# Performance work log

Measured on AMD Instinct MI355X. Metric: run time of the kernel, lower is better.

## Reference

```python
import jax, jax.numpy as jnp
import numpy as np

B, S, D, DM, H, DH, DF, L, T = 4096, 64, 256, 512, 4, 64, 512, 6, 20


def mish(x):
    return x * jnp.tanh(jax.nn.softplus(x))


def layernorm(x, eps=1e-5):
    mu = jnp.mean(x, axis=-1, keepdims=True)
    var = jnp.var(x, axis=-1, keepdims=True)
    return (x - mu) * jax.lax.rsqrt(var + eps)


def setup_inputs() -> dict:
    key = jax.random.key(0)
    ks = iter(jax.random.split(key, 32))
    w = lambda *shape: jax.random.normal(next(ks), shape, dtype=jnp.float32) * 0.02
    inp = {
        'x_t': jax.random.normal(next(ks), (B, S, D), dtype=jnp.float32),
        't': jax.random.randint(next(ks), (B,), 0, T + 1),
        'backbone_latent': jax.random.normal(next(ks), (B, S, DM), dtype=jnp.float32),
        # timestep embedding
        'emb': w(T + 1, D),
        'te_w1': w(D, 4 * D), 'te_b1': jnp.zeros((4 * D,), jnp.float32),
        'te_w2': w(4 * D, D), 'te_b2': jnp.zeros((D,), jnp.float32),
        # cond projection
        'cp_w1': w(DM, D), 'cp_b1': jnp.zeros((D,), jnp.float32),
        'cp_w2': w(D, D), 'cp_b2': jnp.zeros((D,), jnp.float32),
        # stacked per-layer DiT block params [L, ...]
        'adaln_w': w(L, D, 6 * D), 'adaln_b': jnp.zeros((L, 6 * D), jnp.float32),
        'qkv_w': w(L, D, 3 * D), 'qkv_b': jnp.zeros((L, 3 * D), jnp.float32),
        'op_w': w(L, D, D), 'op_b': jnp.zeros((L, D), jnp.float32),
        'ffn_w1': w(L, D, DF), 'ffn_b1': jnp.zeros((L, DF), jnp.float32),
        'ffn_w2': w(L, DF, D), 'ffn_b2': jnp.zeros((L, D), jnp.float32),
        # final adaLN + projection (random here for nontrivial test, zero-init in original)
        'fa_w': w(D, 2 * D), 'fa_b': jnp.zeros((2 * D,), jnp.float32),
        'fp_w': w(D, D), 'fp_b': jnp.zeros((D,), jnp.float32),
    }
    return inp


def _forward(x_t, t, backbone_latent, emb, te_w1, te_b1, te_w2, te_b2,
             cp_w1, cp_b1, cp_w2, cp_b2, adaln_w, adaln_b, qkv_w, qkv_b,
             op_w, op_b, ffn_w1, ffn_b1, ffn_w2, ffn_b2, fa_w, fa_b, fp_w, fp_b):
    # conditioning vector c: [B, D]
    te = emb[t]                                   # [B, D]
    te = mish(te @ te_w1 + te_b1) @ te_w2 + te_b2
    cond = jnp.mean(backbone_latent, axis=1)      # [B, DM]
    cond = mish(cond @ cp_w1 + cp_b1) @ cp_w2 + cp_b2
    c = te + cond
    mc = mish(c)

    x = x_t
    for l in range(L):
        mod = (mc @ adaln_w[l] + adaln_b[l])[:, None, :]   # [B, 1, 6D]
        sh1, sc1, g1, sh2, sc2, g2 = jnp.split(mod, 6, axis=-1)
        # attention sub-block
        h = layernorm(x) * (1.0 + sc1) + sh1
        qkv = (h @ qkv_w[l] + qkv_b[l]).reshape(B, S, 3, H, DH)
        q = qkv[:, :, 0].transpose(0, 2, 1, 3)   # [B, H, S, DH]
        k = qkv[:, :, 1].transpose(0, 2, 1, 3)
        v = qkv[:, :, 2].transpose(0, 2, 1, 3)
        attn = jax.nn.softmax(jnp.einsum('bhsd,bhtd->bhst', q, k) * DH ** -0.5, axis=-1)
        h = jnp.einsum('bhst,bhtd->bhsd', attn, v).transpose(0, 2, 1, 3).reshape(B, S, D)
        h = h @ op_w[l] + op_b[l]
        x = x + g1 * h
        # FFN sub-block
        h = layernorm(x) * (1.0 + sc2) + sh2
        h = mish(h @ ffn_w1[l] + ffn_b1[l]) @ ffn_w2[l] + ffn_b2[l]
        x = x + g2 * h

    mod = (mc @ fa_w + fa_b)[:, None, :]
    shift, scale = jnp.split(mod, 2, axis=-1)
    x = layernorm(x) * (1.0 + scale) + shift
    return x @ fp_w + fp_b


def reference(x_t, t, backbone_latent, emb, te_w1, te_b1, te_w2, te_b2,
              cp_w1, cp_b1, cp_w2, cp_b2, adaln_w, adaln_b, qkv_w, qkv_b,
              op_w, op_b, ffn_w1, ffn_b1, ffn_w2, ffn_b2, fa_w, fa_b, fp_w, fp_b):
    return _forward(x_t, t, backbone_latent, emb, te_w1, te_b1, te_w2, te_b2,
                    cp_w1, cp_b1, cp_w2, cp_b2, adaln_w, adaln_b, qkv_w, qkv_b,
                    op_w, op_b, ffn_w1, ffn_b1, ffn_w2, ffn_b2, fa_w, fa_b, fp_w, fp_b)
```

## Files before the change

kernel.cpp:

```cpp
#include <hip/hip_runtime.h>

typedef unsigned short u16;
typedef float f32x4 __attribute__((ext_vector_type(4)));
typedef __bf16 bf16x8 __attribute__((ext_vector_type(8)));

__device__ __forceinline__ u16 f2b(float f) {
  unsigned u = __builtin_bit_cast(unsigned, f);
  u += 0x7FFF + ((u >> 16) & 1);
  return (u16)(u >> 16);
}

__device__ __forceinline__ float b2f(u16 v) {
  unsigned u = (unsigned)v << 16;
  return __builtin_bit_cast(float, u);
}

__device__ __forceinline__ f32x4 ld_bf4(const u16* p) {
  ushort4 v = *(const ushort4*)p;
  f32x4 r;
  r[0] = b2f(v.x); r[1] = b2f(v.y); r[2] = b2f(v.z); r[3] = b2f(v.w);
  return r;
}

__device__ __forceinline__ float mishf(float x) {
// ... 271 lines not shown
      f32x4 xn = x + g4 * (acc[mt][nt] + b4);
      acc[mt][nt] = xn;
      s1[mt] += xn[0] + xn[1] + xn[2] + xn[3];
      s2[mt] += xn[0] * xn[0] + xn[1] * xn[1] + xn[2] * xn[2] + xn[3] * xn[3];
    }
  }
#pragma unroll
  for (int mt = 0; mt < 4; ++mt) {
    s1[mt] += __shfl_xor(s1[mt], 16); s1[mt] += __shfl_xor(s1[mt], 32);
    s2[mt] += __shfl_xor(s2[mt], 16); s2[mt] += __shfl_xor(s2[mt], 32);
  }
  float* st = (float*)&As[0][0];
  if (lane < 16) {
#pragma unroll
    for (int mt = 0; mt < 4; ++mt) {
      st[wave * 128 + mt * 16 + lane] = s1[mt];
      st[wave * 128 + 64 + mt * 16 + lane] = s2[mt];
    }
  }
  __syncthreads();
  float mean[4], rstd[4];
#pragma unroll
  for (int mt = 0; mt < 4; ++mt) {
    float a = 0.f, q = 0.f;
#pragma unroll
    for (int w2 = 0; w2 < 4; ++w2) {
      a += st[w2 * 128 + mt * 16 + rl];
      q += st[w2 * 128 + 64 + mt * 16 + rl];
    }
    mean[mt] = a * (1.f / 256.f);
    float var = q * (1.f / 256.f) - mean[mt] * mean[mt];
    rstd[mt] = rsqrtf(fmaxf(var, 0.f) + 1e-5f);
  }
#pragma unroll
  for (int nt = 0; nt < 4; ++nt) {
    const int col = wc + nt * 16 + c4;
    const f32x4 sc4 = ld_bf4(lnsc + b * lnstride + col);
    const f32x4 sh4 = ld_bf4(lnsh + b * lnstride + col);
#pragma unroll
    for (int mt = 0; mt < 4; ++mt) {
      const long row = tm + mt * 16 + rl;
      ushort4 xo;
      xo.x = f2b(acc[mt][nt][0]); xo.y = f2b(acc[mt][nt][1]);
      xo.z = f2b(acc[mt][nt][2]); xo.w = f2b(acc[mt][nt][3]);
      *(ushort4*)(xout + row * 256 + col) = xo;
      f32x4 h = (acc[mt][nt] - mean[mt]) * rstd[mt] * (1.f + sc4) + sh4;
      ushort4 o;
      o.x = f2b(h[0]); o.y = f2b(h[1]); o.z = f2b(h[2]); o.w = f2b(h[3]);
      *(ushort4*)(hout + row * 256 + col) = o;
    }
  }
}

__global__ __launch_bounds__(512)
void ffn_fused(const u16* __restrict__ xln, const u16* __restrict__ W1t,
               const float* __restrict__ b1, const u16* __restrict__ W2t,
               const float* __restrict__ b2, const u16* __restrict__ xres,
               const u16* __restrict__ gptr,
               const u16* __restrict__ lnsh, const u16* __restrict__ lnsc, int lnstride,
               u16* __restrict__ xout, u16* __restrict__ hout) {
  __shared__ __align__(16) u16 Ax[64 * 256];
  __shared__ __align__(16) u16 Ws[2][256 * 64];
  __shared__ __align__(16) u16 H1[64 * 512];
  const int tid = threadIdx.x, lane = tid & 63, wave = tid >> 6;
  const long b = blockIdx.x;
  const int rl = lane & 15;
  const int c4 = (lane >> 4) << 2;
  const int kq = lane >> 4;

  {
    const u16* src = xln + b * (64 * 256);
#pragma unroll
    for (int i = 0; i < 4; ++i) {
      int c = tid + (i << 9);
      int r = c >> 5, cc = c & 31;
      int sch = (cc & ~7) | ((cc & 7) ^ (r & 7));
      gl_lds16(src + r * 256 + (sch << 3), &Ax[c << 3]);
    }
  }
  auto stageW = [&](const u16* Wsrc, int Kw, int R0, int k0, int buf) {
#pragma unroll
    for (int i = 0; i < 4; ++i) {
      int c = tid + (i << 9);
      int r = c >> 3;
      int sch = (c & 7) ^ (r & 7);
      gl_lds16(Wsrc + (long)(R0 + r) * Kw + k0 + (sch << 3), &Ws[buf][c << 3]);
    }
  };
  stageW(W1t, 256, 0, 0, 0);
  __syncthreads();

  int cur = 0;
  for (int nh = 0; nh < 2; ++nh) {
    f32x4 acc[4][2] = {};
    for (int t = 0; t < 4; ++t) {
      int s = nh * 4 + t;
      if (s < 7) stageW(W1t, 256, ((s + 1) >> 2) * 256, ((s + 1) & 3) * 64, cur ^ 1);
      else stageW(W2t, 512, 0, 0, cur ^ 1);
#pragma unroll
      for (int kt = 0; kt < 2; ++kt) {
        bf16x8 av[4], bv[2];
#pragma unroll
        for (int mt = 0; mt < 4; ++mt) {
          int r = mt * 16 + rl;
          int kc = t * 8 + kt * 4 + kq;
          int slot = (kc & ~7) | ((kc & 7) ^ (r & 7));
          av[mt] = ldb8(&Ax[r * 256 + (slot << 3)]);
        }
#pragma unroll
        for (int nf = 0; nf < 2; ++nf) {
          int wr_ = wave * 32 + nf * 16 + rl;
          int slot = (kt * 4 + kq) ^ (wr_ & 7);
          bv[nf] = ldb8(&Ws[cur][wr_ * 64 + (slot << 3)]);
        }
#pragma unroll
        for (int mt = 0; mt < 4; ++mt)
#pragma unroll
          for (int nf = 0; nf < 2; ++nf)
            acc[mt][nf] = __builtin_amdgcn_mfma_f32_16x16x32_bf16(bv[nf], av[mt], acc[mt][nf], 0, 0, 0);
      }
      __syncthreads();
      cur ^= 1;
    }
#pragma unroll
    for (int nf = 0; nf < 2; ++nf) {
      const int col = nh * 256 + wave * 32 + nf * 16 + c4;
      const f32x4 bb = *(const f32x4*)(b1 + col);
      const int c8 = col >> 3;
      const int sub = (col & 7) << 1;
#pragma unroll
      for (int mt = 0; mt < 4; ++mt) {
        const int r = mt * 16 + rl;
        f32x4 v = acc[mt][nf] + bb;
        ushort4 o;
        o.x = f2b(mishf(v[0])); o.y = f2b(mishf(v[1]));
        o.z = f2b(mishf(v[2])); o.w = f2b(mishf(v[3]));
        int slot = (c8 & ~7) | ((c8 & 7) ^ (r & 7));
        *(ushort4*)((char*)H1 + r * 1024 + (slot << 4) + sub) = o;
      }
    }
  }
  __syncthreads();

  f32x4 acc[4][2] = {};
  for (int t = 0; t < 8; ++t) {
    if (t < 7) stageW(W2t, 512, 0, (t + 1) * 64, cur ^ 1);
#pragma unroll
    for (int kt = 0; kt < 2; ++kt) {
      bf16x8 av[4], bv[2];
#pragma unroll
      for (int mt = 0; mt < 4; ++mt) {
        int r = mt * 16 + rl;
        int kc = t * 8 + kt * 4 + kq;
        int slot = (kc & ~7) | ((kc & 7) ^ (r & 7));
        av[mt] = ldb8((const u16*)((const char*)H1 + r * 1024 + (slot << 4)));
      }
#pragma unroll
      for (int nf = 0; nf < 2; ++nf) {
        int wr_ = wave * 32 + nf * 16 + rl;
        int slot = (kt * 4 + kq) ^ (wr_ & 7);
        bv[nf] = ldb8(&Ws[cur][wr_ * 64 + (slot << 3)]);
      }
#pragma unroll
      for (int mt = 0; mt < 4; ++mt)
#pragma unroll
        for (int nf = 0; nf < 2; ++nf)
          acc[mt][nf] = __builtin_amdgcn_mfma_f32_16x16x32_bf16(bv[nf], av[mt], acc[mt][nf], 0, 0, 0);
    }
    __syncthreads();
    cur ^= 1;
  }
  float s1[4] = {}, s2[4] = {};
#pragma unroll
  for (int nf = 0; nf < 2; ++nf) {
    const int col = wave * 32 + nf * 16 + c4;
    const f32x4 bb = *(const f32x4*)(b2 + col);
    const f32x4 g4 = ld_bf4(gptr + b * 1536 + col);
#pragma unroll
    for (int mt = 0; mt < 4; ++mt) {
      const long row = b * 64 + mt * 16 + rl;
      f32x4 x = ld_bf4(xres + row * 256 + col);
      f32x4 xn = x + g4 * (acc[mt][nf] + bb);
      acc[mt][nf] = xn;
      s1[mt] += xn[0] + xn[1] + xn[2] + xn[3];
      s2[mt] += xn[0] * xn[0] + xn[1] * xn[1] + xn[2] * xn[2] + xn[3] * xn[3];
    }
  }
#pragma unroll
  for (int mt = 0; mt < 4; ++mt) {
    s1[mt] += __shfl_xor(s1[mt], 16); s1[mt] += __shfl_xor(s1[mt], 32);
    s2[mt] += __shfl_xor(s2[mt], 16); s2[mt] += __shfl_xor(s2[mt], 32);
  }
  float* st = (float*)&Ax[0];
  if (lane < 16) {
#pragma unroll
    for (int mt = 0; mt < 4; ++mt) {
      st[wave * 128 + mt * 16 + lane] = s1[mt];
      st[wave * 128 + 64 + mt * 16 + lane] = s2[mt];
    }
  }
  __syncthreads();
  float mean[4], rstd[4];
#pragma unroll
  for (int mt = 0; mt < 4; ++mt) {
    float a = 0.f, q = 0.f;
#pragma unroll
    for (int w2 = 0; w2 < 8; ++w2) {
      a += st[w2 * 128 + mt * 16 + rl];
      q += st[w2 * 128 + 64 + mt * 16 + rl];
    }
    mean[mt] = a * (1.f / 256.f);
    float var = q * (1.f / 256.f) - mean[mt] * mean[mt];
    rstd[mt] = rsqrtf(fmaxf(var, 0.f) + 1e-5f);
  }
#pragma unroll
  for (int nf = 0; nf < 2; ++nf) {
    const int col = wave * 32 + nf * 16 + c4;
    const f32x4 sc4 = ld_bf4(lnsc + b * lnstride + col);
    const f32x4 sh4 = ld_bf4(lnsh + b * lnstride + col);
#pragma unroll
    for (int mt = 0; mt < 4; ++mt) {
      const long row = b * 64 + mt * 16 + rl;
      ushort4 xo;
      xo.x = f2b(acc[mt][nf][0]); xo.y = f2b(acc[mt][nf][1]);
      xo.z = f2b(acc[mt][nf][2]); xo.w = f2b(acc[mt][nf][3]);
      *(ushort4*)(xout + row * 256 + col) = xo;
      f32x4 h = (acc[mt][nf] - mean[mt]) * rstd[mt] * (1.f + sc4) + sh4;
      ushort4 o;
      o.x = f2b(h[0]); o.y = f2b(h[1]); o.z = f2b(h[2]); o.w = f2b(h[3]);
      *(ushort4*)(hout + row * 256 + col) = o;
    }
  }
}

__global__ __launch_bounds__(128)
void attn_kernel(const u16* __restrict__ qkv, u16* __restrict__ out) {
  __shared__ __align__(16) u16 vt_s[2][64 * 72];
  __shared__ __align__(16) u16 p_s[2][64 * 72];
  const int lane = threadIdx.x & 63;
  const int wave = threadIdx.x >> 6;
  const long b = blockIdx.x >> 1;
  const int h = ((blockIdx.x & 1) << 1) | wave;
  u16* vt = vt_s[wave];
  u16* pl = p_s[wave];
  const u16* base = qkv + b * (64 * 768);
#pragma unroll
  for (int it = 0; it < 8; ++it) {
    int chunk = it * 64 + lane;
    int t = chunk >> 3, dhb = (chunk & 7) << 3;
    union { uint4 u; u16 s[8]; } uv;
    uv.u = *(const uint4*)(base + t * 768 + 512 + h * 64 + dhb);
#pragma unroll
    for (int j = 0; j < 8; ++j) vt[(dhb + j) * 72 + t] = uv.s[j];
  }
  const u16* qb = base + h * 64;
  const u16* kb = base + 256 + h * 64;
  f32x4 sacc[4][4] = {};
#pragma unroll
  for (int kt = 0; kt < 2; ++kt) {
    bf16x8 qa[4], kv[4];
#pragma unroll
    for (int mt = 0; mt < 4; ++mt)
      qa[mt] = ldb8(qb + ((lane & 15) + mt * 16) * 768 + kt * 32 + ((lane >> 4) << 3));
#pragma unroll
    for (int nt = 0; nt < 4; ++nt)
      kv[nt] = ldb8(kb + ((lane & 15) + nt * 16) * 768 + kt * 32 + ((lane >> 4) << 3));
#pragma unroll
    for (int mt = 0; mt < 4; ++mt)
#pragma unroll
      for (int nt = 0; nt < 4; ++nt)
        sacc[mt][nt] = __builtin_amdgcn_mfma_f32_16x16x32_bf16(qa[mt], kv[nt], sacc[mt][nt], 0, 0, 0);
  }
  const float scale = 0.125f;
#pragma unroll
  for (int mt = 0; mt < 4; ++mt) {
#pragma unroll
    for (int r = 0; r < 4; ++r) {
      float mx = fmaxf(fmaxf(sacc[mt][0][r], sacc[mt][1][r]), fmaxf(sacc[mt][2][r], sacc[mt][3][r]));
#pragma unroll
      for (int m = 1; m <= 8; m <<= 1) mx = fmaxf(mx, __shfl_xor(mx, m));
      float p[4];
      float sum = 0.f;
#pragma unroll
      for (int nt = 0; nt < 4; ++nt) { p[nt] = __expf((sacc[mt][nt][r] - mx) * scale); sum += p[nt]; }
#pragma unroll
      for (int m = 1; m <= 8; m <<= 1) sum += __shfl_xor(sum, m);
      const float rinv = 1.f / sum;
      const int s = mt * 16 + ((lane >> 4) << 2) + r;
#pragma unroll
      for (int nt = 0; nt < 4; ++nt) pl[s * 72 + nt * 16 + (lane & 15)] = f2b(p[nt] * rinv);
    }
  }
  __syncthreads();
  f32x4 oacc[4][4] = {};
#pragma unroll
  for (int kt = 0; kt < 2; ++kt) {
    bf16x8 pa[4], vv[4];
#pragma unroll
    for (int mt = 0; mt < 4; ++mt)
      pa[mt] = ldb8(pl + ((lane & 15) + mt * 16) * 72 + kt * 32 + ((lane >> 4) << 3));
#pragma unroll
    for (int nt = 0; nt < 4; ++nt)
      vv[nt] = ldb8(vt + ((lane & 15) + nt * 16) * 72 + kt * 32 + ((lane >> 4) << 3));
#pragma unroll
    for (int mt = 0; mt < 4; ++mt)
#pragma unroll
      for (int nt = 0; nt < 4; ++nt)
        oacc[mt][nt] = __builtin_amdgcn_mfma_f32_16x16x32_bf16(vv[nt], pa[mt], oacc[mt][nt], 0, 0, 0);
  }
  u16* ob = out + b * (64 * 256) + h * 64;
#pragma unroll
  for (int mt = 0; mt < 4; ++mt)
#pragma unroll
    for (int nt = 0; nt < 4; ++nt) {
      const int s = mt * 16 + (lane & 15);
      const int d4 = nt * 16 + ((lane >> 4) << 2);
      ushort4 o;
      o.x = f2b(oacc[mt][nt][0]); o.y = f2b(oacc[mt][nt][1]);
      o.z = f2b(oacc[mt][nt][2]); o.w = f2b(oacc[mt][nt][3]);
      *(ushort4*)(ob + s * 256 + d4) = o;
    }
}

extern "C" void kernel_launch(void* const* d_in, const int* in_sizes, int n_in,
                              void* d_out, int out_size, void* d_ws, size_t ws_size,
                              hipStream_t stream) {
  (void)in_sizes; (void)n_in; (void)out_size; (void)ws_size;
  const int B = 4096, L = 6;
  const long BSr = (long)B * 64;

  const float* x_t = (const float*)d_in[0];
  const int* tvec = (const int*)d_in[1];
  const float* backbone = (const float*)d_in[2];
  const float* emb = (const float*)d_in[3];
  const float* te_w1 = (const float*)d_in[4];
  const float* te_b1 = (const float*)d_in[5];
  const float* te_w2 = (const float*)d_in[6];
  const float* te_b2 = (const float*)d_in[7];
  const float* cp_w1 = (const float*)d_in[8];
  const float* cp_b1 = (const float*)d_in[9];
  const float* cp_w2 = (const float*)d_in[10];
  const float* cp_b2 = (const float*)d_in[11];
  const float* adaln_w = (const float*)d_in[12];
  const float* adaln_b = (const float*)d_in[13];
  const float* qkv_w = (const float*)d_in[14];
  const float* qkv_b = (const float*)d_in[15];
  const float* op_w = (const float*)d_in[16];
  const float* op_b = (const float*)d_in[17];
  const float* ffn_w1 = (const float*)d_in[18];
  const float* ffn_b1 = (const float*)d_in[19];
  const float* ffn_w2 = (const float*)d_in[20];
  const float* ffn_b2 = (const float*)d_in[21];
  const float* fa_w = (const float*)d_in[22];
  const float* fa_b = (const float*)d_in[23];
  const float* fp_w = (const float*)d_in[24];
  const float* fp_b = (const float*)d_in[25];

  char* w = (char*)d_ws;
  auto alloc = [&](size_t bytes) { char* p = w; w += (bytes + 255) & ~(size_t)255; return p; };
  u16* WT_cp1 = (u16*)alloc(256L * 512 * 2);
  u16* WT_cp2 = (u16*)alloc(256L * 256 * 2);
  u16* WT_adaln = (u16*)alloc(6L * 1536 * 256 * 2);
  u16* WT_qkv = (u16*)alloc(6L * 768 * 256 * 2);
  u16* WT_op = (u16*)alloc(6L * 256 * 256 * 2);
  u16* WT_f1 = (u16*)alloc(6L * 512 * 256 * 2);
  u16* WT_f2 = (u16*)alloc(6L * 256 * 512 * 2);
  u16* WT_fa = (u16*)alloc(512L * 256 * 2);
  u16* WT_fp = (u16*)alloc(256L * 256 * 2);
  float* te_tab = (float*)alloc(21L * 256 * 4);
  u16* cond = (u16*)alloc(4096L * 512 * 2);
  u16* c1 = (u16*)alloc(4096L * 256 * 2);
  u16* mc = (u16*)alloc(4096L * 256 * 2);
  u16* modb6 = (u16*)alloc(6L * 4096 * 1536 * 2);
  u16* famod = (u16*)alloc(4096L * 512 * 2);
  u16* hbuf = (u16*)alloc(BSr * 256 * 2);
  u16* qkvbuf = (u16*)alloc(BSr * 768 * 2);
  u16* xbuf = (u16*)d_out;

  transpose_w<<<dim3(4, 8, 1), 256, 0, stream>>>(cp_w1, WT_cp1, 512, 256);
  transpose_w<<<dim3(4, 4, 1), 256, 0, stream>>>(cp_w2, WT_cp2, 256, 256);
  transpose_w<<<dim3(24, 4, 6), 256, 0, stream>>>(adaln_w, WT_adaln, 256, 1536);
  transpose_w<<<dim3(12, 4, 6), 256, 0, stream>>>(qkv_w, WT_qkv, 256, 768);
  transpose_w<<<dim3(4, 4, 6), 256, 0, stream>>>(op_w, WT_op, 256, 256);
  transpose_w<<<dim3(8, 4, 6), 256, 0, stream>>>(ffn_w1, WT_f1, 256, 512);
  transpose_w<<<dim3(4, 8, 6), 256, 0, stream>>>(ffn_w2, WT_f2, 512, 256);
  transpose_w<<<dim3(8, 4, 1), 256, 0, stream>>>(fa_w, WT_fa, 256, 512);
  transpose_w<<<dim3(4, 4, 1), 256, 0, stream>>>(fp_w, WT_fp, 256, 256);

  te_table_kernel<<<21, 1024, 0, stream>>>(emb, te_w1, te_b1, te_w2, te_b2, te_tab);
  cond_mean_kernel<<<4096, 256, 0, stream>>>(backbone, cond);

  gemm_bt<1><<<dim3(2, 32), 256, 0, stream>>>(cond, WT_cp1, cp_b1, c1, nullptr, nullptr, 4096, 256, 512);
  gemm_bt<4><<<dim3(2, 32), 256, 0, stream>>>(c1, WT_cp2, cp_b2, mc, tvec, te_tab, 4096, 256, 256);
  gemm_bt<0><<<dim3(4, 32), 256, 0, stream>>>(mc, WT_fa, fa_b, famod, nullptr, nullptr, 4096, 512, 256);
  for (int l = 0; l < L; ++l)
    gemm_bt<0><<<dim3(12, 32), 256, 0, stream>>>(mc, WT_adaln + (long)l * 1536 * 256, adaln_b + l * 1536,
                                                 modb6 + (long)l * 4096 * 1536, nullptr, nullptr, 4096, 1536, 256);

  ln_mod<<<BSr / 4, 256, 0, stream>>>(x_t, modb6, 1536, 0, 256, hbuf);

  for (int l = 0; l < L; ++l) {
    const u16* mb = modb6 + (long)l * 4096 * 1536;
    gemm_bt<0><<<dim3(6, BSr / 128), 256, 0, stream>>>(hbuf, WT_qkv + (long)l * 768 * 256, qkv_b + l * 768,
                                                       qkvbuf, nullptr, nullptr, (int)BSr, 768, 256);
    attn_kernel<<<B * 2, 128, 0, stream>>>(qkvbuf, hbuf);
    if (l == 0)
      gemm_ln<256, true><<<BSr / 64, 256, 0, stream>>>(hbuf, WT_op, op_b, x_t, mb + 512,
                                                       mb + 768, mb + 1024, 1536, xbuf, hbuf);
    else
      gemm_ln<256, false><<<BSr / 64, 256, 0, stream>>>(hbuf, WT_op + (long)l * 256 * 256, op_b + l * 256,
                                                        xbuf, mb + 512, mb + 768, mb + 1024, 1536, xbuf, hbuf);
    const u16* nsh = (l < 5) ? (modb6 + (long)(l + 1) * 4096 * 1536) : famod;
    const u16* nsc = (l < 5) ? (modb6 + (long)(l + 1) * 4096 * 1536 + 256) : (famod + 256);
    const int nstride = (l < 5) ? 1536 : 512;
    ffn_fused<<<B, 512, 0, stream>>>(hbuf, WT_f1 + (long)l * 512 * 256, ffn_b1 + l * 512,
                                     WT_f2 + (long)l * 256 * 512, ffn_b2 + l * 256,
                                     xbuf, mb + 1280, nsh, nsc, nstride, xbuf, hbuf);
  }
  gemm_bt<3><<<dim3(2, BSr / 128), 256, 0, stream>>>(hbuf, WT_fp, fp_b, d_out, nullptr, nullptr, (int)BSr, 256, 256);
}
```

Measured before the change: 6.485 ms.

## Fuse QKV projection with attention and retile FFN to 32-row blocks

Adds a qkv_attn kernel that computes the QKV projection for two heads of one batch element straight into shared memory and then runs softmax attention there. This removes the qkvbuf round trip through global memory and one launch per layer. The FFN kernel is also restructured to handle 32 rows per 256-thread block with a single-buffered weight tile, doubling the grid and cutting shared memory use so more blocks can be resident. The cost is that each QKV block re-reads the input rows, the attention path leaves two of six waves idle, and weight staging in the FFN no longer overlaps with compute.

```diff
diff --git a/kernel.cpp b/kernel.cpp
--- a/kernel.cpp
+++ b/kernel.cpp
@@ -347,274 +347,354 @@
   }
 }
 
-__global__ __launch_bounds__(512)
+__global__ __launch_bounds__(384)
+void qkv_attn(const u16* __restrict__ xln, const u16* __restrict__ Wq,
+              const float* __restrict__ qbias, u16* __restrict__ aout) {
+  __shared__ __align__(16) u16 Wlds[384 * 32];
+  __shared__ __align__(16) u16 QP[2][64 * 64];
+  __shared__ __align__(16) u16 Kl[2][64 * 64];
+  __shared__ __align__(16) u16 Vt[128 * 64];
+  const int tid = threadIdx.x, lane = tid & 63, wave = tid >> 6;
+  const long b = blockIdx.x >> 1;
+  const int hp = blockIdx.x & 1;
+  const int rl = lane & 15, kq = lane >> 4, c4 = kq << 2;
+  const u16* xg = xln + b * (64 * 256);
+
+  f32x4 acc[4][4] = {};
+  for (int t = 0; t < 8; ++t) {
+    {
+      const int k0 = t << 5;
+#pragma unroll
+      for (int i = 0; i < 4; ++i) {
+        int c = tid + i * 384;
+        int r = c >> 2, kcl = c & 3;
+        int sch = kcl ^ ((r >> 1) & 3);
+        long rg = (long)((r >> 7) * 256 + hp * 128 + (r & 127));
+        gl_lds16(Wq + rg * 256 + k0 + (sch << 3), &Wlds[c << 3]);
+      }
+    }
+    __syncthreads();
+    bf16x8 av[4], bv[4];
+#pragma unroll
+    for (int mt = 0; mt < 4; ++mt)
+      av[mt] = ldb8(xg + (mt * 16 + rl) * 256 + (t << 5) + (kq << 3));
+#pragma unroll
+    for (int nt = 0; nt < 4; ++nt) {
+      const int wr_ = (wave << 6) + nt * 16 + rl;
+      const int slot = kq ^ ((wr_ >> 1) & 3);
+      bv[nt] = ldb8(&Wlds[(wr_ << 5) + (slot << 3)]);
+    }
+    if (wave < 4) {
+#pragma unroll
+      for (int mt = 0; mt < 4; ++mt)
+#pragma unroll
+        for (int nt = 0; nt < 4; ++nt)
+          acc[mt][nt] = __builtin_amdgcn_mfma_f32_16x16x32_bf16(bv[nt], av[mt], acc[mt][nt], 0, 0, 0);
+    } else {
+#pragma unroll
+      for (int mt = 0; mt < 4; ++mt)
+#pragma unroll
+        for (int nt = 0; nt < 4; ++nt)
+          acc[mt][nt] = __builtin_amdgcn_mfma_f32_16x16x32_bf16(av[mt], bv[nt], acc[mt][nt], 0, 0, 0);
+    }
+    __syncthreads();
+  }
+  if (wave < 4) {
+    const int head = wave & 1;
+    u16* dst = (wave >> 1) ? Kl[head] : QP[head];
+#pragma unroll
+    for (int nt = 0; nt < 4; ++nt) {
+      const int dh = nt * 16 + c4;
+      const int gc = (wave >> 1) * 256 + hp * 128 + (wave & 1) * 64 + dh;
+      const f32x4 bb = *(const f32x4*)(qbias + gc);
+      const int c16 = dh >> 3, sub = (dh & 7) << 1;
+#pragma unroll
+      for (int mt = 0; mt < 4; ++mt) {
+        const int tok = mt * 16 + rl;
+        f32x4 v = acc[mt][nt] + bb;
+        ushort4 o;
+        o.x = f2b(v[0]); o.y = f2b(v[1]); o.z = f2b(v[2]); o.w = f2b(v[3]);
+        const int slot = c16 ^ (tok & 7);
+        *(ushort4*)((char*)dst + tok * 128 + (slot << 4) + sub) = o;
+      }
+    }
+  } else {
+#pragma unroll
+    for (int nt = 0; nt < 4; ++nt) {
+      const int dh = ((wave - 4) << 6) + nt * 16 + rl;
+      const float bb = qbias[512 + hp * 128 + dh];
+#pragma unroll
+      for (int mt = 0; mt < 4; ++mt) {
+        const int tok = mt * 16 + c4;
+        f32x4 v = acc[mt][nt] + bb;
+        ushort4 o;
+        o.x = f2b(v[0]); o.y = f2b(v[1]); o.z = f2b(v[2]); o.w = f2b(v[3]);
+        const int c16 = tok >> 3, sub = (tok & 7) << 1;
+        const int slot = c16 ^ (dh & 7);
+        *(ushort4*)((char*)Vt + dh * 128 + (slot << 4) + sub) = o;
+      }
+    }
+  }
+  __syncthreads();
+
+  const int ah = wave >> 1, arow = (wave & 1) << 5;
+  f32x4 sacc[2][4] = {};
+  if (wave < 4) {
+#pragma unroll
+    for (int kt = 0; kt < 2; ++kt) {
+      const int kc = kt * 4 + kq;
+      bf16x8 qa[2], kv[4];
+#pragma unroll
+      for (int mt = 0; mt < 2; ++mt) {
+        const int q = arow + mt * 16 + rl;
+        qa[mt] = ldb8((const u16*)((char*)QP[ah] + q * 128 + ((kc ^ (q & 7)) << 4)));
+      }
+#pragma unroll
+      for (int nt = 0; nt < 4; ++nt) {
+        const int tt = nt * 16 + rl;
+        kv[nt] = ldb8((const u16*)((char*)Kl[ah] + tt * 128 + ((kc ^ (tt & 7)) << 4)));
+      }
+#pragma unroll
+      for (int mt = 0; mt < 2; ++mt)
+#pragma unroll
+        for (int nt = 0; nt < 4; ++nt)
+          sacc[mt][nt] = __builtin_amdgcn_mfma_f32_16x16x32_bf16(kv[nt], qa[mt], sacc[mt][nt], 0, 0, 0);
+    }
+  }
+  __syncthreads();
+  if (wave < 4) {
+    const float scale = 0.125f;
+#pragma unroll
+    for (int mt = 0; mt < 2; ++mt) {
+      float mx = -1e30f;
+#pragma unroll
+      for (int nt = 0; nt < 4; ++nt)
+#pragma unroll
+        for (int j = 0; j < 4; ++j) mx = fmaxf(mx, sacc[mt][nt][j]);
+      mx = fmaxf(mx, __shfl_xor(mx, 16));
+      mx = fmaxf(mx, __shfl_xor(mx, 32));
+      float sum = 0.f;
+      f32x4 p[4];
+#pragma unroll
+      for (int nt = 0; nt < 4; ++nt)
+#pragma unroll
+        for (int j = 0; j < 4; ++j) { p[nt][j] = __expf((sacc[mt][nt][j] - mx) * scale); sum += p[nt][j]; }
+      sum += __shfl_xor(sum, 16);
+      sum += __shfl_xor(sum, 32);
+      const float rinv = 1.f / sum;
+      const int q = arow + mt * 16 + rl;
+#pragma unroll
+      for (int nt = 0; nt < 4; ++nt) {
+        const int tcol = nt * 16 + c4;
+        ushort4 o;
+        o.x = f2b(p[nt][0] * rinv); o.y = f2b(p[nt][1] * rinv);
+        o.z = f2b(p[nt][2] * rinv); o.w = f2b(p[nt][3] * rinv);
+        const int slot = (tcol >> 3) ^ (q & 7);
+        *(ushort4*)((char*)QP[ah] + q * 128 + (slot << 4) + ((tcol & 7) << 1)) = o;
+      }
+    }
+  }
+  __syncthreads();
+  if (wave < 4) {
+    f32x4 oacc[2][4] = {};
+#pragma unroll
+    for (int kt = 0; kt < 2; ++kt) {
+      const int kc = kt * 4 + kq;
+      bf16x8 pa[2], vv[4];
+#pragma unroll
+      for (int mt = 0; mt < 2; ++mt) {
+        const int q = arow + mt * 16 + rl;
+        pa[mt] = ldb8((const u16*)((char*)QP[ah] + q * 128 + ((kc ^ (q & 7)) << 4)));
+      }
+#pragma unroll
+      for (int nt = 0; nt < 4; ++nt) {
+        const int dh = (ah << 6) + nt * 16 + rl;
+        vv[nt] = ldb8((const u16*)((char*)Vt + dh * 128 + ((kc ^ (dh & 7)) << 4)));
+      }
+#pragma unroll
+      for (int mt = 0; mt < 2; ++mt)
+#pragma unroll
+        for (int nt = 0; nt < 4; ++nt)
+          oacc[mt][nt] = __builtin_amdgcn_mfma_f32_16x16x32_bf16(vv[nt], pa[mt], oacc[mt][nt], 0, 0, 0);
+    }
+    u16* ob = aout + b * (64 * 256) + (hp * 2 + ah) * 64;
+#pragma unroll
+    for (int mt = 0; mt < 2; ++mt)
+#pragma unroll
+      for (int nt = 0; nt < 4; ++nt) {
+        const int q = arow + mt * 16 + rl;
+        const int dh = nt * 16 + c4;
+        ushort4 o;
+        o.x = f2b(oacc[mt][nt][0]); o.y = f2b(oacc[mt][nt][1]);
+        o.z = f2b(oacc[mt][nt][2]); o.w = f2b(oacc[mt][nt][3]);
+        *(ushort4*)(ob + q * 256 + dh) = o;
+      }
+  }
+}
+
+__global__ __launch_bounds__(256)
 void ffn_fused(const u16* __restrict__ xln, const u16* __restrict__ W1t,
                const float* __restrict__ b1, const u16* __restrict__ W2t,
                const float* __restrict__ b2, const u16* __restrict__ xres,
                const u16* __restrict__ gptr,
                const u16* __restrict__ lnsh, const u16* __restrict__ lnsc, int lnstride,
                u16* __restrict__ xout, u16* __restrict__ hout) {
-  __shared__ __align__(16) u16 Ax[64 * 256];
-  __shared__ __align__(16) u16 Ws[2][256 * 64];
-  __shared__ __align__(16) u16 H1[64 * 512];
+  __shared__ __align__(16) u16 Ax[32 * 256];
+  __shared__ __align__(16) u16 Ws[256 * 64];
+  __shared__ __align__(16) u16 H1[32 * 512];
   const int tid = threadIdx.x, lane = tid & 63, wave = tid >> 6;
-  const long b = blockIdx.x;
-  const int rl = lane & 15;
-  const int c4 = (lane >> 4) << 2;
-  const int kq = lane >> 4;
+  const long blk = blockIdx.x;
+  const long b = blk >> 1;
+  const long row0 = blk << 5;
+  const int rl = lane & 15, kq = lane >> 4, c4 = kq << 2;
 
   {
-    const u16* src = xln + b * (64 * 256);
+    const u16* src = xln + row0 * 256;
 #pragma unroll
     for (int i = 0; i < 4; ++i) {
-      int c = tid + (i << 9);
+      int c = tid + (i << 8);
       int r = c >> 5, cc = c & 31;
       int sch = (cc & ~7) | ((cc & 7) ^ (r & 7));
       gl_lds16(src + r * 256 + (sch << 3), &Ax[c << 3]);
     }
   }
-  auto stageW = [&](const u16* Wsrc, int Kw, int R0, int k0, int buf) {
-#pragma unroll
-    for (int i = 0; i < 4; ++i) {
-      int c = tid + (i << 9);
+  auto stageW = [&](int s) {
+    const u16* Wsrc; int Kw, R0, k0;
+    if (s < 8) { Wsrc = W1t; Kw = 256; R0 = (s >> 2) << 8; k0 = (s & 3) << 6; }
+    else       { Wsrc = W2t; Kw = 512; R0 = 0;             k0 = (s - 8) << 6; }
+#pragma unroll
+    for (int i = 0; i < 8; ++i) {
+      int c = tid + (i << 8);
       int r = c >> 3;
       int sch = (c & 7) ^ (r & 7);
-      gl_lds16(Wsrc + (long)(R0 + r) * Kw + k0 + (sch << 3), &Ws[buf][c << 3]);
+      gl_lds16(Wsrc + (long)(R0 + r) * Kw + k0 + (sch << 3), &Ws[c << 3]);
     }
   };
-  stageW(W1t, 256, 0, 0, 0);
-  __syncthreads();
-
-  int cur = 0;
-  for (int nh = 0; nh < 2; ++nh) {
-    f32x4 acc[4][2] = {};
-    for (int t = 0; t < 4; ++t) {
-      int s = nh * 4 + t;
-      if (s < 7) stageW(W1t, 256, ((s + 1) >> 2) * 256, ((s + 1) & 3) * 64, cur ^ 1);
-      else stageW(W2t, 512, 0, 0, cur ^ 1);
-#pragma unroll
-      for (int kt = 0; kt < 2; ++kt) {
-        bf16x8 av[4], bv[2];
-#pragma unroll
-        for (int mt = 0; mt < 4; ++mt) {
-          int r = mt * 16 + rl;
-          int kc = t * 8 + kt * 4 + kq;
-          int slot = (kc & ~7) | ((kc & 7) ^ (r & 7));
-          av[mt] = ldb8(&Ax[r * 256 + (slot << 3)]);
+  stageW(0);
+  __syncthreads();
+
+  f32x4 acc[2][4] = {};
+  for (int s = 0; s < 16; ++s) {
+#pragma unroll
+    for (int kt = 0; kt < 2; ++kt) {
+      bf16x8 av[2], bv[4];
+      if (s < 8) {
+        const int kc = (s & 3) * 8 + kt * 4 + kq;
+#pragma unroll
+        for (int mt = 0; mt < 2; ++mt) {
+          const int r = mt * 16 + rl;
+          const int slot = (kc & ~7) | ((kc & 7) ^ (r & 7));
+          av[mt] = ldb8(&Ax[(r << 8) + (slot << 3)]);
         }
-#pragma unroll
-        for (int nf = 0; nf < 2; ++nf) {
-          int wr_ = wave * 32 + nf * 16 + rl;
-          int slot = (kt * 4 + kq) ^ (wr_ & 7);
-          bv[nf] = ldb8(&Ws[cur][wr_ * 64 + (slot << 3)]);
+      } else {
+        const int kc = (s - 8) * 8 + kt * 4 + kq;
+#pragma unroll
+        for (int mt = 0; mt < 2; ++mt) {
+          const int r = mt * 16 + rl;
+          const int slot = (kc & ~7) | ((kc & 7) ^ (r & 7));
+          av[mt] = ldb8(&H1[(r << 9) + (slot << 3)]);
         }
-#pragma unroll
-        for (int mt = 0; mt < 4; ++mt)
-#pragma unroll
-          for (int nf = 0; nf < 2; ++nf)
-            acc[mt][nf] = __builtin_amdgcn_mfma_f32_16x16x32_bf16(bv[nf], av[mt], acc[mt][nf], 0, 0, 0);
-      }
-      __syncthreads();
-      cur ^= 1;
-    }
-#pragma unroll
-    for (int nf = 0; nf < 2; ++nf) {
-      const int col = nh * 256 + wave * 32 + nf * 16 + c4;
-      const f32x4 bb = *(const f32x4*)(b1 + col);
-      const int c8 = col >> 3;
-      const int sub = (col & 7) << 1;
-#pragma unroll
-      for (int mt = 0; mt < 4; ++mt) {
-        const int r = mt * 16 + rl;
-        f32x4 v = acc[mt][nf] + bb;
-        ushort4 o;
-        o.x = f2b(mishf(v[0])); o.y = f2b(mishf(v[1]));
-        o.z = f2b(mishf(v[2])); o.w = f2b(mishf(v[3]));
-        int slot = (c8 & ~7) | ((c8 & 7) ^ (r & 7));
-        *(ushort4*)((char*)H1 + r * 1024 + (slot << 4) + sub) = o;
-      }
-    }
-  }
-  __syncthreads();
-
-  f32x4 acc[4][2] = {};
-  for (int t = 0; t < 8; ++t) {
-    if (t < 7) stageW(W2t, 512, 0, (t + 1) * 64, cur ^ 1);
-#pragma unroll
-    for (int kt = 0; kt < 2; ++kt) {
-      bf16x8 av[4], bv[2];
-#pragma unroll
-      for (int mt = 0; mt < 4; ++mt) {
-        int r = mt * 16 + rl;
-        int kc = t * 8 + kt * 4 + kq;
-        int slot = (kc & ~7) | ((kc & 7) ^ (r & 7));
-        av[mt] = ldb8((const u16*)((const char*)H1 + r * 1024 + (slot << 4)));
-      }
-#pragma unroll
-      for (int nf = 0; nf < 2; ++nf) {
-        int wr_ = wave * 32 + nf * 16 + rl;
-        int slot = (kt * 4 + kq) ^ (wr_ & 7);
-        bv[nf] = ldb8(&Ws[cur][wr_ * 64 + (slot << 3)]);
-      }
-#pragma unroll
-      for (int mt = 0; mt < 4; ++mt)
-#pragma unroll
-        for (int nf = 0; nf < 2; ++nf)
-          acc[mt][nf] = __builtin_amdgcn_mfma_f32_16x16x32_bf16(bv[nf], av[mt], acc[mt][nf], 0, 0, 0);
+      }
+#pragma unroll
+      for (int nt = 0; nt < 4; ++nt) {
+        const int wr_ = (wave << 6) + nt * 16 + rl;
+        const int slot = (kt * 4 + kq) ^ (wr_ & 7);
+        bv[nt] = ldb8(&Ws[(wr_ << 6) + (slot << 3)]);
+      }
+#pragma unroll
+      for (int mt = 0; mt < 2; ++mt)
+#pragma unroll
+        for (int nt = 0; nt < 4; ++nt)
+          acc[mt][nt] = __builtin_amdgcn_mfma_f32_16x16x32_bf16(bv[nt], av[mt], acc[mt][nt], 0, 0, 0);
     }
     __syncthreads();
-    cur ^= 1;
-  }
-  float s1[4] = {}, s2[4] = {};
-#pragma unroll
-  for (int nf = 0; nf < 2; ++nf) {
-    const int col = wave * 32 + nf * 16 + c4;
+    if (s == 3 || s == 7) {
+      const int nh = s >> 2;
+#pragma unroll
+      for (int nt = 0; nt < 4; ++nt) {
+        const int col = (nh << 8) + (wave << 6) + nt * 16 + c4;
+        const f32x4 bb = *(const f32x4*)(b1 + col);
+        const int c16 = col >> 3, sub = (col & 7) << 1;
+#pragma unroll
+        for (int mt = 0; mt < 2; ++mt) {
+          const int r = mt * 16 + rl;
+          f32x4 v = acc[mt][nt] + bb;
+          ushort4 o;
+          o.x = f2b(mishf(v[0])); o.y = f2b(mishf(v[1]));
+          o.z = f2b(mishf(v[2])); o.w = f2b(mishf(v[3]));
+          const int slot = (c16 & ~7) | ((c16 & 7) ^ (r & 7));
+          *(ushort4*)((char*)H1 + r * 1024 + (slot << 4) + sub) = o;
+        }
+      }
+#pragma unroll
+      for (int mt = 0; mt < 2; ++mt)
+#pragma unroll
+        for (int nt = 0; nt < 4; ++nt) acc[mt][nt] = (f32x4){0.f, 0.f, 0.f, 0.f};
+    }
+    if (s < 15) { stageW(s + 1); __syncthreads(); }
+  }
+
+  float s1[2] = {}, s2[2] = {};
+#pragma unroll
+  for (int nt = 0; nt < 4; ++nt) {
+    const int col = (wave << 6) + nt * 16 + c4;
     const f32x4 bb = *(const f32x4*)(b2 + col);
     const f32x4 g4 = ld_bf4(gptr + b * 1536 + col);
 #pragma unroll
-    for (int mt = 0; mt < 4; ++mt) {
-      const long row = b * 64 + mt * 16 + rl;
+    for (int mt = 0; mt < 2; ++mt) {
+      const long row = row0 + mt * 16 + rl;
       f32x4 x = ld_bf4(xres + row * 256 + col);
-      f32x4 xn = x + g4 * (acc[mt][nf] + bb);
-      acc[mt][nf] = xn;
+      f32x4 xn = x + g4 * (acc[mt][nt] + bb);
+      acc[mt][nt] = xn;
       s1[mt] += xn[0] + xn[1] + xn[2] + xn[3];
       s2[mt] += xn[0] * xn[0] + xn[1] * xn[1] + xn[2] * xn[2] + xn[3] * xn[3];
     }
   }
 #pragma unroll
-  for (int mt = 0; mt < 4; ++mt) {
+  for (int mt = 0; mt < 2; ++mt) {
     s1[mt] += __shfl_xor(s1[mt], 16); s1[mt] += __shfl_xor(s1[mt], 32);
     s2[mt] += __shfl_xor(s2[mt], 16); s2[mt] += __shfl_xor(s2[mt], 32);
   }
   float* st = (float*)&Ax[0];
   if (lane < 16) {
 #pragma unroll
-    for (int mt = 0; mt < 4; ++mt) {
-      st[wave * 128 + mt * 16 + lane] = s1[mt];
-      st[wave * 128 + 64 + mt * 16 + lane] = s2[mt];
-    }
-  }
-  __syncthreads();
-  float mean[4], rstd[4];
-#pragma unroll
-  for (int mt = 0; mt < 4; ++mt) {
+    for (int mt = 0; mt < 2; ++mt) {
+      st[wave * 64 + mt * 16 + lane] = s1[mt];
+      st[256 + wave * 64 + mt * 16 + lane] = s2[mt];
+    }
+  }
+  __syncthreads();
+  float mean[2], rstd[2];
+#pragma unroll
+  for (int mt = 0; mt < 2; ++mt) {
     float a = 0.f, q = 0.f;
 #pragma unroll
-    for (int w2 = 0; w2 < 8; ++w2) {
-      a += st[w2 * 128 + mt * 16 + rl];
-      q += st[w2 * 128 + 64 + mt * 16 + rl];
+    for (int w2 = 0; w2 < 4; ++w2) {
+      a += st[w2 * 64 + mt * 16 + rl];
+      q += st[256 + w2 * 64 + mt * 16 + rl];
     }
     mean[mt] = a * (1.f / 256.f);
     float var = q * (1.f / 256.f) - mean[mt] * mean[mt];
     rstd[mt] = rsqrtf(fmaxf(var, 0.f) + 1e-5f);
   }
 #pragma unroll
-  for (int nf = 0; nf < 2; ++nf) {
-    const int col = wave * 32 + nf * 16 + c4;
+  for (int nt = 0; nt < 4; ++nt) {
+    const int col = (wave << 6) + nt * 16 + c4;
     const f32x4 sc4 = ld_bf4(lnsc + b * lnstride + col);
     const f32x4 sh4 = ld_bf4(lnsh + b * lnstride + col);
 #pragma unroll
-    for (int mt = 0; mt < 4; ++mt) {
-      const long row = b * 64 + mt * 16 + rl;
+    for (int mt = 0; mt < 2; ++mt) {
+      const long row = row0 + mt * 16 + rl;
       ushort4 xo;
-      xo.x = f2b(acc[mt][nf][0]); xo.y = f2b(acc[mt][nf][1]);
-      xo.z = f2b(acc[mt][nf][2]); xo.w = f2b(acc[mt][nf][3]);
+      xo.x = f2b(acc[mt][nt][0]); xo.y = f2b(acc[mt][nt][1]);
+      xo.z = f2b(acc[mt][nt][2]); xo.w = f2b(acc[mt][nt][3]);
       *(ushort4*)(xout + row * 256 + col) = xo;
-      f32x4 h = (acc[mt][nf] - mean[mt]) * rstd[mt] * (1.f + sc4) + sh4;
+      f32x4 h = (acc[mt][nt] - mean[mt]) * rstd[mt] * (1.f + sc4) + sh4;
       ushort4 o;
       o.x = f2b(h[0]); o.y = f2b(h[1]); o.z = f2b(h[2]); o.w = f2b(h[3]);
       *(ushort4*)(hout + row * 256 + col) = o;
     }
   }
-}
-
-__global__ __launch_bounds__(128)
-void attn_kernel(const u16* __restrict__ qkv, u16* __restrict__ out) {
-  __shared__ __align__(16) u16 vt_s[2][64 * 72];
-  __shared__ __align__(16) u16 p_s[2][64 * 72];
-  const int lane = threadIdx.x & 63;
-  const int wave = threadIdx.x >> 6;
-  const long b = blockIdx.x >> 1;
-  const int h = ((blockIdx.x & 1) << 1) | wave;
-  u16* vt = vt_s[wave];
-  u16* pl = p_s[wave];
-  const u16* base = qkv + b * (64 * 768);
-#pragma unroll
-  for (int it = 0; it < 8; ++it) {
-    int chunk = it * 64 + lane;
-    int t = chunk >> 3, dhb = (chunk & 7) << 3;
-    union { uint4 u; u16 s[8]; } uv;
-    uv.u = *(const uint4*)(base + t * 768 + 512 + h * 64 + dhb);
-#pragma unroll
-    for (int j = 0; j < 8; ++j) vt[(dhb + j) * 72 + t] = uv.s[j];
-  }
-  const u16* qb = base + h * 64;
-  const u16* kb = base + 256 + h * 64;
-  f32x4 sacc[4][4] = {};
-#pragma unroll
-  for (int kt = 0; kt < 2; ++kt) {
-    bf16x8 qa[4], kv[4];
-#pragma unroll
-    for (int mt = 0; mt < 4; ++mt)
-      qa[mt] = ldb8(qb + ((lane & 15) + mt * 16) * 768 + kt * 32 + ((lane >> 4) << 3));
-#pragma unroll
-    for (int nt = 0; nt < 4; ++nt)
-      kv[nt] = ldb8(kb + ((lane & 15) + nt * 16) * 768 + kt * 32 + ((lane >> 4) << 3));
-#pragma unroll
-    for (int mt = 0; mt < 4; ++mt)
-#pragma unroll
-      for (int nt = 0; nt < 4; ++nt)
-        sacc[mt][nt] = __builtin_amdgcn_mfma_f32_16x16x32_bf16(qa[mt], kv[nt], sacc[mt][nt], 0, 0, 0);
-  }
-  const float scale = 0.125f;
-#pragma unroll
-  for (int mt = 0; mt < 4; ++mt) {
-#pragma unroll
-    for (int r = 0; r < 4; ++r) {
-      float mx = fmaxf(fmaxf(sacc[mt][0][r], sacc[mt][1][r]), fmaxf(sacc[mt][2][r], sacc[mt][3][r]));
-#pragma unroll
-      for (int m = 1; m <= 8; m <<= 1) mx = fmaxf(mx, __shfl_xor(mx, m));
-      float p[4];
-      float sum = 0.f;
-#pragma unroll
-      for (int nt = 0; nt < 4; ++nt) { p[nt] = __expf((sacc[mt][nt][r] - mx) * scale); sum += p[nt]; }
-#pragma unroll
-      for (int m = 1; m <= 8; m <<= 1) sum += __shfl_xor(sum, m);
-      const float rinv = 1.f / sum;
-      const int s = mt * 16 + ((lane >> 4) << 2) + r;
-#pragma unroll
-      for (int nt = 0; nt < 4; ++nt) pl[s * 72 + nt * 16 + (lane & 15)] = f2b(p[nt] * rinv);
-    }
-  }
-  __syncthreads();
-  f32x4 oacc[4][4] = {};
-#pragma unroll
-  for (int kt = 0; kt < 2; ++kt) {
-    bf16x8 pa[4], vv[4];
-#pragma unroll
-    for (int mt = 0; mt < 4; ++mt)
-      pa[mt] = ldb8(pl + ((lane & 15) + mt * 16) * 72 + kt * 32 + ((lane >> 4) << 3));
-#pragma unroll
-    for (int nt = 0; nt < 4; ++nt)
-      vv[nt] = ldb8(vt + ((lane & 15) + nt * 16) * 72 + kt * 32 + ((lane >> 4) << 3));
-#pragma unroll
-    for (int mt = 0; mt < 4; ++mt)
-#pragma unroll
-      for (int nt = 0; nt < 4; ++nt)
-        oacc[mt][nt] = __builtin_amdgcn_mfma_f32_16x16x32_bf16(vv[nt], pa[mt], oacc[mt][nt], 0, 0, 0);
-  }
-  u16* ob = out + b * (64 * 256) + h * 64;
-#pragma unroll
-  for (int mt = 0; mt < 4; ++mt)
-#pragma unroll
-    for (int nt = 0; nt < 4; ++nt) {
-      const int s = mt * 16 + (lane & 15);
-      const int d4 = nt * 16 + ((lane >> 4) << 2);
-      ushort4 o;
-      o.x = f2b(oacc[mt][nt][0]); o.y = f2b(oacc[mt][nt][1]);
-      o.z = f2b(oacc[mt][nt][2]); o.w = f2b(oacc[mt][nt][3]);
-      *(ushort4*)(ob + s * 256 + d4) = o;
-    }
 }
 
 extern "C" void kernel_launch(void* const* d_in, const int* in_sizes, int n_in,
@@ -696,21 +776,19 @@
 
   for (int l = 0; l < L; ++l) {
     const u16* mb = modb6 + (long)l * 4096 * 1536;
-    gemm_bt<0><<<dim3(6, BSr / 128), 256, 0, stream>>>(hbuf, WT_qkv + (long)l * 768 * 256, qkv_b + l * 768,
-                                                       qkvbuf, nullptr, nullptr, (int)BSr, 768, 256);
-    attn_kernel<<<B * 2, 128, 0, stream>>>(qkvbuf, hbuf);
+    qkv_attn<<<B * 2, 384, 0, stream>>>(hbuf, WT_qkv + (long)l * 768 * 256, qkv_b + l * 768, qkvbuf);
     if (l == 0)
-      gemm_ln<256, true><<<BSr / 64, 256, 0, stream>>>(hbuf, WT_op, op_b, x_t, mb + 512,
+      gemm_ln<256, true><<<BSr / 64, 256, 0, stream>>>(qkvbuf, WT_op, op_b, x_t, mb + 512,
                                                        mb + 768, mb + 1024, 1536, xbuf, hbuf);
     else
-      gemm_ln<256, false><<<BSr / 64, 256, 0, stream>>>(hbuf, WT_op + (long)l * 256 * 256, op_b + l * 256,
+      gemm_ln<256, false><<<BSr / 64, 256, 0, stream>>>(qkvbuf, WT_op + (long)l * 256 * 256, op_b + l * 256,
                                                         xbuf, mb + 512, mb + 768, mb + 1024, 1536, xbuf, hbuf);
     const u16* nsh = (l < 5) ? (modb6 + (long)(l + 1) * 4096 * 1536) : famod;
     const u16* nsc = (l < 5) ? (modb6 + (long)(l + 1) * 4096 * 1536 + 256) : (famod + 256);
     const int nstride = (l < 5) ? 1536 : 512;
-    ffn_fused<<<B, 512, 0, stream>>>(hbuf, WT_f1 + (long)l * 512 * 256, ffn_b1 + l * 512,
-                                     WT_f2 + (long)l * 256 * 512, ffn_b2 + l * 256,
-                                     xbuf, mb + 1280, nsh, nsc, nstride, xbuf, hbuf);
+    ffn_fused<<<BSr / 32, 256, 0, stream>>>(hbuf, WT_f1 + (long)l * 512 * 256, ffn_b1 + l * 512,
+                                            WT_f2 + (long)l * 256 * 512, ffn_b2 + l * 256,
+                                            xbuf, mb + 1280, nsh, nsc, nstride, xbuf, hbuf);
   }
   gemm_bt<3><<<dim3(2, BSr / 128), 256, 0, stream>>>(hbuf, WT_fp, fp_b, d_out, nullptr, nullptr, (int)BSr, 256, 256);
 }
```

Measured after the change: 7.045 ms. +8.6%, slower.

## Restructure fused FFN first GEMM to read activations from global and drop LDS A tile

Applied to the files above, without the earlier changes.

The first FFN GEMM no longer stages the 64x256 activation tile in shared memory. Each wave now reads A fragments straight from global memory and covers 64 output columns (a 4x4 accumulator tile) in one pass over K, with W1 streamed in 32-wide K chunks. Removing the 32KB A buffer cuts LDS use per block, which may allow more resident blocks, and it drops the two-half N loop. The cost is repeated uncoalesced global or L2 reads of activations across waves, plus more accumulator registers per wave.

```diff
diff --git a/kernel.cpp b/kernel.cpp
--- a/kernel.cpp
+++ b/kernel.cpp
@@ -354,129 +354,118 @@
                const u16* __restrict__ gptr,
                const u16* __restrict__ lnsh, const u16* __restrict__ lnsc, int lnstride,
                u16* __restrict__ xout, u16* __restrict__ hout) {
-  __shared__ __align__(16) u16 Ax[64 * 256];
-  __shared__ __align__(16) u16 Ws[2][256 * 64];
+  __shared__ __align__(16) u16 Ws[2][512 * 32];
   __shared__ __align__(16) u16 H1[64 * 512];
   const int tid = threadIdx.x, lane = tid & 63, wave = tid >> 6;
   const long b = blockIdx.x;
-  const int rl = lane & 15;
-  const int c4 = (lane >> 4) << 2;
-  const int kq = lane >> 4;
-
-  {
-    const u16* src = xln + b * (64 * 256);
+  const long row0 = b << 6;
+  const int rl = lane & 15, kq = lane >> 4, c4 = kq << 2;
+  const u16* xg = xln + row0 * 256;
+
+  auto stageA = [&](int t, int buf) {
 #pragma unroll
     for (int i = 0; i < 4; ++i) {
       int c = tid + (i << 9);
-      int r = c >> 5, cc = c & 31;
-      int sch = (cc & ~7) | ((cc & 7) ^ (r & 7));
-      gl_lds16(src + r * 256 + (sch << 3), &Ax[c << 3]);
-    }
-  }
-  auto stageW = [&](const u16* Wsrc, int Kw, int R0, int k0, int buf) {
+      int r = c >> 2, kcl = c & 3;
+      int sch = kcl ^ ((r >> 1) & 3);
+      gl_lds16(W1t + (long)r * 256 + (t << 5) + (sch << 3), &Ws[buf][c << 3]);
+    }
+  };
+  auto stageB = [&](int t, int buf) {
 #pragma unroll
     for (int i = 0; i < 4; ++i) {
       int c = tid + (i << 9);
       int r = c >> 3;
       int sch = (c & 7) ^ (r & 7);
-      gl_lds16(Wsrc + (long)(R0 + r) * Kw + k0 + (sch << 3), &Ws[buf][c << 3]);
+      gl_lds16(W2t + (long)r * 512 + (t << 6) + (sch << 3), &Ws[buf][c << 3]);
     }
   };
-  stageW(W1t, 256, 0, 0, 0);
-  __syncthreads();
-
+
+  stageA(0, 0);
+  __syncthreads();
   int cur = 0;
-  for (int nh = 0; nh < 2; ++nh) {
-    f32x4 acc[4][2] = {};
-    for (int t = 0; t < 4; ++t) {
-      int s = nh * 4 + t;
-      if (s < 7) stageW(W1t, 256, ((s + 1) >> 2) * 256, ((s + 1) & 3) * 64, cur ^ 1);
-      else stageW(W2t, 512, 0, 0, cur ^ 1);
-#pragma unroll
-      for (int kt = 0; kt < 2; ++kt) {
-        bf16x8 av[4], bv[2];
-#pragma unroll
-        for (int mt = 0; mt < 4; ++mt) {
-          int r = mt * 16 + rl;
-          int kc = t * 8 + kt * 4 + kq;
-          int slot = (kc & ~7) | ((kc & 7) ^ (r & 7));
-          av[mt] = ldb8(&Ax[r * 256 + (slot << 3)]);
-        }
-#pragma unroll
-        for (int nf = 0; nf < 2; ++nf) {
-          int wr_ = wave * 32 + nf * 16 + rl;
-          int slot = (kt * 4 + kq) ^ (wr_ & 7);
-          bv[nf] = ldb8(&Ws[cur][wr_ * 64 + (slot << 3)]);
-        }
-#pragma unroll
-        for (int mt = 0; mt < 4; ++mt)
-#pragma unroll
-          for (int nf = 0; nf < 2; ++nf)
-            acc[mt][nf] = __builtin_amdgcn_mfma_f32_16x16x32_bf16(bv[nf], av[mt], acc[mt][nf], 0, 0, 0);
-      }
-      __syncthreads();
-      cur ^= 1;
-    }
-#pragma unroll
-    for (int nf = 0; nf < 2; ++nf) {
-      const int col = nh * 256 + wave * 32 + nf * 16 + c4;
-      const f32x4 bb = *(const f32x4*)(b1 + col);
-      const int c8 = col >> 3;
-      const int sub = (col & 7) << 1;
+
+  f32x4 acc[4][4] = {};
+  for (int t = 0; t < 8; ++t) {
+    if (t < 7) stageA(t + 1, cur ^ 1);
+    else stageB(0, cur ^ 1);
+    bf16x8 av[4], bv[4];
+#pragma unroll
+    for (int mt = 0; mt < 4; ++mt)
+      av[mt] = ldb8(xg + (mt * 16 + rl) * 256 + (t << 5) + (kq << 3));
+#pragma unroll
+    for (int nt = 0; nt < 4; ++nt) {
+      const int wr_ = (wave << 6) + nt * 16 + rl;
+      const int slot = kq ^ ((wr_ >> 1) & 3);
+      bv[nt] = ldb8(&Ws[cur][(wr_ << 5) + (slot << 3)]);
+    }
+#pragma unroll
+    for (int mt = 0; mt < 4; ++mt)
+#pragma unroll
+      for (int nt = 0; nt < 4; ++nt)
+        acc[mt][nt] = __builtin_amdgcn_mfma_f32_16x16x32_bf16(bv[nt], av[mt], acc[mt][nt], 0, 0, 0);
+    __syncthreads();
+    cur ^= 1;
+  }
+#pragma unroll
+  for (int nt = 0; nt < 4; ++nt) {
+    const int col = (wave << 6) + nt * 16 + c4;
+    const f32x4 bb = *(const f32x4*)(b1 + col);
+    const int c16 = col >> 3, sub = (col & 7) << 1;
+#pragma unroll
+    for (int mt = 0; mt < 4; ++mt) {
+      const int r = mt * 16 + rl;
+      f32x4 v = acc[mt][nt] + bb;
+      ushort4 o;
+      o.x = f2b(mishf(v[0])); o.y = f2b(mishf(v[1]));
+      o.z = f2b(mishf(v[2])); o.w = f2b(mishf(v[3]));
+      const int slot = (c16 & ~7) | ((c16 & 7) ^ (r & 7));
+      *(ushort4*)((char*)H1 + r * 1024 + (slot << 4) + sub) = o;
+    }
+  }
+  __syncthreads();
+
+  f32x4 accB[4][2] = {};
+  for (int t = 0; t < 8; ++t) {
+    if (t < 7) stageB(t + 1, cur ^ 1);
+#pragma unroll
+    for (int kt = 0; kt < 2; ++kt) {
+      const int kc = (t << 3) + (kt << 2) + kq;
+      bf16x8 av[4], bv[2];
 #pragma unroll
       for (int mt = 0; mt < 4; ++mt) {
         const int r = mt * 16 + rl;
-        f32x4 v = acc[mt][nf] + bb;
-        ushort4 o;
-        o.x = f2b(mishf(v[0])); o.y = f2b(mishf(v[1]));
-        o.z = f2b(mishf(v[2])); o.w = f2b(mishf(v[3]));
-        int slot = (c8 & ~7) | ((c8 & 7) ^ (r & 7));
-        *(ushort4*)((char*)H1 + r * 1024 + (slot << 4) + sub) = o;
-      }
-    }
-  }
-  __syncthreads();
-
-  f32x4 acc[4][2] = {};
-  for (int t = 0; t < 8; ++t) {
-    if (t < 7) stageW(W2t, 512, 0, (t + 1) * 64, cur ^ 1);
-#pragma unroll
-    for (int kt = 0; kt < 2; ++kt) {
-      bf16x8 av[4], bv[2];
-#pragma unroll
-      for (int mt = 0; mt < 4; ++mt) {
-        int r = mt * 16 + rl;
-        int kc = t * 8 + kt * 4 + kq;
-        int slot = (kc & ~7) | ((kc & 7) ^ (r & 7));
+        const int slot = (kc & ~7) | ((kc & 7) ^ (r & 7));
         av[mt] = ldb8((const u16*)((const char*)H1 + r * 1024 + (slot << 4)));
       }
 #pragma unroll
       for (int nf = 0; nf < 2; ++nf) {
-        int wr_ = wave * 32 + nf * 16 + rl;
-        int slot = (kt * 4 + kq) ^ (wr_ & 7);
-        bv[nf] = ldb8(&Ws[cur][wr_ * 64 + (slot << 3)]);
+        const int wr_ = (wave << 5) + nf * 16 + rl;
+        const int slot = ((kt << 2) + kq) ^ (wr_ & 7);
+        bv[nf] = ldb8(&Ws[cur][(wr_ << 6) + (slot << 3)]);
       }
 #pragma unroll
       for (int mt = 0; mt < 4; ++mt)
 #pragma unroll
         for (int nf = 0; nf < 2; ++nf)
-          acc[mt][nf] = __builtin_amdgcn_mfma_f32_16x16x32_bf16(bv[nf], av[mt], acc[mt][nf], 0, 0, 0);
+          accB[mt][nf] = __builtin_amdgcn_mfma_f32_16x16x32_bf16(bv[nf], av[mt], accB[mt][nf], 0, 0, 0);
     }
     __syncthreads();
     cur ^= 1;
   }
+
   float s1[4] = {}, s2[4] = {};
 #pragma unroll
   for (int nf = 0; nf < 2; ++nf) {
-    const int col = wave * 32 + nf * 16 + c4;
+    const int col = (wave << 5) + nf * 16 + c4;
     const f32x4 bb = *(const f32x4*)(b2 + col);
     const f32x4 g4 = ld_bf4(gptr + b * 1536 + col);
 #pragma unroll
     for (int mt = 0; mt < 4; ++mt) {
-      const long row = b * 64 + mt * 16 + rl;
+      const long row = row0 + mt * 16 + rl;
       f32x4 x = ld_bf4(xres + row * 256 + col);
-      f32x4 xn = x + g4 * (acc[mt][nf] + bb);
-      acc[mt][nf] = xn;
+      f32x4 xn = x + g4 * (accB[mt][nf] + bb);
+      accB[mt][nf] = xn;
       s1[mt] += xn[0] + xn[1] + xn[2] + xn[3];
       s2[mt] += xn[0] * xn[0] + xn[1] * xn[1] + xn[2] * xn[2] + xn[3] * xn[3];
     }
@@ -486,7 +475,7 @@
     s1[mt] += __shfl_xor(s1[mt], 16); s1[mt] += __shfl_xor(s1[mt], 32);
     s2[mt] += __shfl_xor(s2[mt], 16); s2[mt] += __shfl_xor(s2[mt], 32);
   }
-  float* st = (float*)&Ax[0];
+  float* st = (float*)&H1[0];
   if (lane < 16) {
 #pragma unroll
     for (int mt = 0; mt < 4; ++mt) {
@@ -510,17 +499,17 @@
   }
 #pragma unroll
   for (int nf = 0; nf < 2; ++nf) {
-    const int col = wave * 32 + nf * 16 + c4;
+    const int col = (wave << 5) + nf * 16 + c4;
     const f32x4 sc4 = ld_bf4(lnsc + b * lnstride + col);
     const f32x4 sh4 = ld_bf4(lnsh + b * lnstride + col);
 #pragma unroll
     for (int mt = 0; mt < 4; ++mt) {
-      const long row = b * 64 + mt * 16 + rl;
+      const long row = row0 + mt * 16 + rl;
       ushort4 xo;
-      xo.x = f2b(acc[mt][nf][0]); xo.y = f2b(acc[mt][nf][1]);
-      xo.z = f2b(acc[mt][nf][2]); xo.w = f2b(acc[mt][nf][3]);
+      xo.x = f2b(accB[mt][nf][0]); xo.y = f2b(accB[mt][nf][1]);
+      xo.z = f2b(accB[mt][nf][2]); xo.w = f2b(accB[mt][nf][3]);
       *(ushort4*)(xout + row * 256 + col) = xo;
-      f32x4 h = (acc[mt][nf] - mean[mt]) * rstd[mt] * (1.f + sc4) + sh4;
+      f32x4 h = (accB[mt][nf] - mean[mt]) * rstd[mt] * (1.f + sc4) + sh4;
       ushort4 o;
       o.x = f2b(h[0]); o.y = f2b(h[1]); o.z = f2b(h[2]); o.w = f2b(h[3]);
       *(ushort4*)(hout + row * 256 + col) = o;
@@ -708,9 +697,9 @@
     const u16* nsh = (l < 5) ? (modb6 + (long)(l + 1) * 4096 * 1536) : famod;
     const u16* nsc = (l < 5) ? (modb6 + (long)(l + 1) * 4096 * 1536 + 256) : (famod + 256);
     const int nstride = (l < 5) ? 1536 : 512;
-    ffn_fused<<<B, 512, 0, stream>>>(hbuf, WT_f1 + (long)l * 512 * 256, ffn_b1 + l * 512,
-                                     WT_f2 + (long)l * 256 * 512, ffn_b2 + l * 256,
-                                     xbuf, mb + 1280, nsh, nsc, nstride, xbuf, hbuf);
+    ffn_fused<<<BSr / 64, 512, 0, stream>>>(hbuf, WT_f1 + (long)l * 512 * 256, ffn_b1 + l * 512,
+                                            WT_f2 + (long)l * 256 * 512, ffn_b2 + l * 256,
+                                            xbuf, mb + 1280, nsh, nsc, nstride, xbuf, hbuf);
   }
   gemm_bt<3><<<dim3(2, BSr / 128), 256, 0, stream>>>(hbuf, WT_fp, fp_b, d_out, nullptr, nullptr, (int)BSr, 256, 256);
 }
```

New measurement: 6.771 ms. +4.4%, slower.
